# Performance work log

Hardware: AMD Instinct MI355X
Metric: run time of the kernel (lower is better)

The kernel has to match this reference:

```python
import jax, jax.numpy as jnp
import numpy as np
from jax import lax

B, T, C = 64, 512, 512  # time_step == channel required by LayerNorm([T, C]) on [B, C, T]
T2 = T // 2  # downsampled length for scale 1 (conv kernel=2, stride=2)
LN_EPS = 1e-5


def _hardswish(x):
    return x * jnp.clip(x + 3.0, 0.0, 6.0) / 6.0


def _triu_mix(z, W, b):
    # TriU: out[..., i] = Linear_i(z[..., 0:i+1]) == causal lower-triangular mixing
    # z: [B, C, T'], W: [T', T'] (row i holds weights of linear i), b: [T']
    mask = jnp.tril(jnp.ones(W.shape, z.dtype))
    return jnp.einsum('bcj,ij->bci', z, W * mask) + b


def setup_inputs() -> dict:
    key = jax.random.key(0)
    ks = jax.random.split(key, 13)
    s = 0.02
    return {
        'x': jax.random.normal(ks[0], (B, T, C), jnp.float32),
        'ln_gamma': jnp.ones((T, C), jnp.float32),
        'ln_beta': jnp.zeros((T, C), jnp.float32),
        'w1': jax.random.normal(ks[1], (T, T), jnp.float32) * s,
        'b1': jax.random.normal(ks[2], (T,), jnp.float32) * s,
        'w2': jax.random.normal(ks[3], (T, T), jnp.float32) * s,
        'b2': jax.random.normal(ks[4], (T,), jnp.float32) * s,
        'conv_w': jax.random.normal(ks[5], (C, C, 2), jnp.float32) * s,  # OIH
        'conv_b': jax.random.normal(ks[6], (C,), jnp.float32) * s,
        'w3': jax.random.normal(ks[7], (T2, T2), jnp.float32) * s,
        'b3': jax.random.normal(ks[8], (T2,), jnp.float32) * s,
        'w4': jax.random.normal(ks[9], (T2, T2), jnp.float32) * s,
        'b4': jax.random.normal(ks[10], (T2,), jnp.float32) * s,
    }


def reference(x, ln_gamma, ln_beta, w1, b1, w2, b2, conv_w, conv_b, w3, b3, w4, b4):
    xp = jnp.transpose(x, (0, 2, 1))  # [B, C, T]
    # scale 0: LayerNorm over last two dims (C, T jointly), affine weight [T, C] == [C, T] positionally
    mean = jnp.mean(xp, axis=(-2, -1), keepdims=True)
    var = jnp.var(xp, axis=(-2, -1), keepdims=True)
    xn = (xp - mean) / jnp.sqrt(var + LN_EPS) * ln_gamma + ln_beta
    y = _triu_mix(xn, w1, b1)
    y = _hardswish(y)
    y = _triu_mix(y, w2, b2)
    # scale 1: Conv1d(C, C, kernel=2, stride=2) then TriU/Hardswish/TriU on length T/2
    z = lax.conv_general_dilated(xp, conv_w, window_strides=(2,), padding='VALID',
                                 dimension_numbers=('NCH', 'OIH', 'NCH'))
    z = z + conv_b[None, :, None]
    z = _triu_mix(z, w3, b3)
    z = _hardswish(z)
    z = _triu_mix(z, w4, b4)
    return jnp.concatenate([y, z], axis=-1)  # [B, C, T + T/2]
```

## Files before the change

### kernel.cpp

```cpp
#include <hip/hip_runtime.h>
#include <hip/hip_bf16.h>


#define NB 64

typedef __bf16 bf16x8 __attribute__((ext_vector_type(8)));
typedef __bf16 bf16x4 __attribute__((ext_vector_type(4)));
typedef float f32x4 __attribute__((ext_vector_type(4)));

#define AS_GLOBAL __attribute__((address_space(1)))
#define AS_LDS    __attribute__((address_space(3)))

__global__ void pre1_k(const float* __restrict__ x, float* __restrict__ part,
                       const float* __restrict__ w1, const float* __restrict__ w2,
                       const float* __restrict__ w3, const float* __restrict__ w4,
                       const float* __restrict__ cw,
                       __bf16* __restrict__ w1b, __bf16* __restrict__ w2b,
                       __bf16* __restrict__ w3b, __bf16* __restrict__ w4b,
                       __bf16* __restrict__ WtT) {
  if (blockIdx.x < 256) {
    int bb = blockIdx.x;
    int b = bb >> 2, q = bb & 3;
    const float4* xb = (const float4*)(x + (size_t)b * 262144 + (size_t)q * 65536);
    float s = 0.f, ss = 0.f;
    for (int it = 0; it < 64; ++it) {
      float4 v = xb[threadIdx.x + 256 * it];
      s += (v.x + v.y) + (v.z + v.w);
      ss += (v.x * v.x + v.y * v.y) + (v.z * v.z + v.w * v.w);
    }
    __shared__ float ls[256], lss[256];
    ls[threadIdx.x] = s; lss[threadIdx.x] = ss;
    __syncthreads();
    for (int off = 128; off > 0; off >>= 1) {
      if (threadIdx.x < off) {
        ls[threadIdx.x] += ls[threadIdx.x + off];
        lss[threadIdx.x] += lss[threadIdx.x + off];
      }
      __syncthreads();
    }
    if (threadIdx.x == 0) { part[bb * 2] = ls[0]; part[bb * 2 + 1] = lss[0]; }
    return;
  }
  int idx = (blockIdx.x - 256) * 256 + threadIdx.x;
  if (idx < 262144) { int i = idx >> 9, j = idx & 511; w1b[idx] = (__bf16)(j <= i ? w1[idx] : 0.f); return; }
  idx -= 262144;
  if (idx < 262144) { int i = idx >> 9, j = idx & 511; w2b[idx] = (__bf16)(j <= i ? w2[idx] : 0.f); return; }
  idx -= 262144;
  if (idx < 65536) { int i = idx >> 8, j = idx & 255; w3b[idx] = (__bf16)(j <= i ? w3[idx] : 0.f); return; }
  idx -= 65536;
  if (idx < 65536) { int i = idx >> 8, j = idx & 255; w4b[idx] = (__bf16)(j <= i ? w4[idx] : 0.f); return; }
  idx -= 65536;
  int o = idx >> 10, r = idx & 1023;
  int i = r & 511, k = r >> 9;
  WtT[idx] = (__bf16)cw[(size_t)o * 1024 + i * 2 + k];
}

__global__ void stats_final_k(const float* __restrict__ part, float* __restrict__ stats) {
  int b = threadIdx.x;
  if (b < NB) {
    float s = 0.f, ss = 0.f;
    for (int q = 0; q < 4; ++q) { s += part[(b * 4 + q) * 2]; ss += part[(b * 4 + q) * 2 + 1]; }
    float mean = s * (1.f / 262144.f);
    float var = ss * (1.f / 262144.f) - mean * mean;
    stats[b * 2] = mean;
    stats[b * 2 + 1] = rsqrtf(var + 1e-5f);
  }
}

__global__ __launch_bounds__(256) void norm_trans_k(
    const float* __restrict__ x, const float* __restrict__ g,
    const float* __restrict__ be, const float* __restrict__ stats,
    __bf16* __restrict__ XnT, __bf16* __restrict__ xbf) {
  __shared__ float ls[64][65];
  int b = blockIdx.z;
  int bc = blockIdx.x * 64;
  int bt = blockIdx.y * 64;
  int tid = threadIdx.x;
  float mean = stats[b * 2], istd = stats[b * 2 + 1];
  const float* xb = x + (size_t)b * 262144;
  __bf16* xo = xbf + (size_t)b * 262144;
  int r0 = tid >> 4;
  int c4 = (tid & 15) * 4;
#pragma unroll
  for (int p = 0; p < 4; ++p) {
    int t = p * 16 + r0;
    float4 v = *(const float4*)&xb[(size_t)(bt + t) * 512 + bc + c4];
    ls[t][c4] = v.x; ls[t][c4 + 1] = v.y; ls[t][c4 + 2] = v.z; ls[t][c4 + 3] = v.w;
    bf16x4 o;
    o[0] = (__bf16)v.x; o[1] = (__bf16)v.y; o[2] = (__bf16)v.z; o[3] = (__bf16)v.w;
    *(bf16x4*)&xo[(size_t)(bt + t) * 512 + bc + c4] = o;
  }
  __syncthreads();
  int cr = tid >> 3;
  int t0 = (tid & 7) * 8;
  __bf16* xnb = XnT + (size_t)b * 262144;
#pragma unroll
  for (int p = 0; p < 2; ++p) {
    int cg = bc + p * 32 + cr;
    int cl = p * 32 + cr;
    float4 g0 = *(const float4*)&g[(size_t)cg * 512 + bt + t0];
    float4 g1 = *(const float4*)&g[(size_t)cg * 512 + bt + t0 + 4];
    float4 e0 = *(const float4*)&be[(size_t)cg * 512 + bt + t0];
    float4 e1 = *(const float4*)&be[(size_t)cg * 512 + bt + t0 + 4];
    float gv[8] = {g0.x, g0.y, g0.z, g0.w, g1.x, g1.y, g1.z, g1.w};
    float ev[8] = {e0.x, e0.y, e0.z, e0.w, e1.x, e1.y, e1.z, e1.w};
    bf16x8 o;
#pragma unroll
    for (int j = 0; j < 8; ++j) {
      float xh = (ls[t0 + j][cl] - mean) * istd;
      o[j] = (__bf16)(xh * gv[j] + ev[j]);
    }
    *(bf16x8*)&xnb[(size_t)cg * 512 + bt + t0] = o;
  }
}

template <int LGX, bool HSW, bool ROWB, bool COLB, bool OUTBF>
__global__ __launch_bounds__(256, 3) void gemm_mfma_k(
    const __bf16* __restrict__ A, long sAb,
    const __bf16* __restrict__ Bt, long sBb,
    void* __restrict__ Cm, long sCb,
    const float* __restrict__ bias,
    int K, int ldc, int c_off) {
  __shared__ __align__(16) __bf16 As[128 * 64];
  __shared__ __align__(16) __bf16 Bs[128 * 64];
  const int tid = threadIdx.x;
  const int lane = tid & 63, wid = tid >> 6;
  const int wm = (wid >> 1) * 64, wn = (wid & 1) * 64;
  const int lr = lane & 15, lg = lane >> 4;

  const int bid = blockIdx.x + (blockIdx.y << LGX) + (blockIdx.z << (LGX + 2));
  const int nid = ((bid & 7) << (LGX + 5)) | (bid >> 3);
  const int bm = (nid & ((1 << LGX) - 1)) * 128;
  const int bn = ((nid >> LGX) & 3) * 128;
  const int bz = nid >> (LGX + 2);

  const int srg = lane >> 3;
  const int ssrc = ((lane & 7) ^ srg) << 3;

  const __bf16* gA[4];
  const __bf16* gB[4];
#pragma unroll
  for (int p = 0; p < 4; ++p) {
    int row = p * 32 + wid * 8 + srg;
    gA[p] = A + (size_t)bz * sAb + (size_t)(bm + row) * K + ssrc;
    gB[p] = Bt + (size_t)bz * sBb + (size_t)(bn + row) * K + ssrc;
  }

  f32x4 acc[4][4] = {};

  for (int k0 = 0; k0 < K; k0 += 64) {
#pragma unroll
    for (int p = 0; p < 4; ++p) {
      __builtin_amdgcn_global_load_lds(
          (const AS_GLOBAL void*)gA[p],
          (AS_LDS void*)&As[(p * 32 + wid * 8) * 64], 16, 0, 0);
      __builtin_amdgcn_global_load_lds(
          (const AS_GLOBAL void*)gB[p],
          (AS_LDS void*)&Bs[(p * 32 + wid * 8) * 64], 16, 0, 0);
      gA[p] += 64;
      gB[p] += 64;
    }
    __syncthreads();
#pragma unroll
    for (int kk = 0; kk < 64; kk += 32) {
      bf16x8 af[4], bfv[4];
#pragma unroll
      for (int f = 0; f < 4; ++f) {
        int ar = wm + f * 16 + lr;
        af[f] = *(const bf16x8*)&As[ar * 64 + ((kk + lg * 8) ^ ((ar & 7) << 3))];
        int br = wn + f * 16 + lr;
        bfv[f] = *(const bf16x8*)&Bs[br * 64 + ((kk + lg * 8) ^ ((br & 7) << 3))];
      }
#pragma unroll
      for (int i = 0; i < 4; ++i)
#pragma unroll
        for (int j = 0; j < 4; ++j)
          acc[i][j] = __builtin_amdgcn_mfma_f32_16x16x32_bf16(af[i], bfv[j], acc[i][j], 0, 0, 0);
    }
    __syncthreads();
  }

#pragma unroll
  for (int i = 0; i < 4; ++i) {
    int row0 = bm + wm + i * 16 + lg * 4;
    float rb0 = 0.f, rb1 = 0.f, rb2 = 0.f, rb3 = 0.f;
    if (ROWB) { rb0 = bias[row0]; rb1 = bias[row0 + 1]; rb2 = bias[row0 + 2]; rb3 = bias[row0 + 3]; }
#pragma unroll
    for (int j = 0; j < 4; ++j) {
      int col = bn + wn + j * 16 + lr;
      float cbv = COLB ? bias[col] : 0.f;
      float v[4] = {acc[i][j][0] + rb0 + cbv, acc[i][j][1] + rb1 + cbv,
                    acc[i][j][2] + rb2 + cbv, acc[i][j][3] + rb3 + cbv};
      if (HSW) {
#pragma unroll
        for (int r = 0; r < 4; ++r) {
          float u = fminf(fmaxf(v[r] + 3.f, 0.f), 6.f);
          v[r] = v[r] * u * (1.f / 6.f);
        }
      }
      if (OUTBF) {
        __bf16* C = (__bf16*)Cm + (size_t)bz * sCb;
        bf16x4 o;
        o[0] = (__bf16)v[0]; o[1] = (__bf16)v[1]; o[2] = (__bf16)v[2]; o[3] = (__bf16)v[3];
        *(bf16x4*)&C[(size_t)col * ldc + c_off + row0] = o;
      } else {
        float* C = (float*)Cm + (size_t)bz * sCb;
        *(float4*)&C[(size_t)col * ldc + c_off + row0] =
            make_float4(v[0], v[1], v[2], v[3]);
      }
    }
  }
}

extern "C" void kernel_launch(void* const* d_in, const int* in_sizes, int n_in,
                              void* d_out, int out_size, void* d_ws, size_t ws_size,
                              hipStream_t stream) {
  const float* x  = (const float*)d_in[0];
  const float* g  = (const float*)d_in[1];
  const float* be = (const float*)d_in[2];
  const float* w1 = (const float*)d_in[3];
  const float* b1 = (const float*)d_in[4];
  const float* w2 = (const float*)d_in[5];
  const float* b2 = (const float*)d_in[6];
  const float* cw = (const float*)d_in[7];
  const float* cb = (const float*)d_in[8];
  const float* w3 = (const float*)d_in[9];
  const float* b3 = (const float*)d_in[10];
  const float* w4 = (const float*)d_in[11];
  const float* b4 = (const float*)d_in[12];
  float* out = (float*)d_out;

  char* ws = (char*)d_ws;
  float*  stats = (float*)(ws);
  float*  part  = (float*)(ws + 4096);
  __bf16* w1b   = (__bf16*)(ws + (1 << 20));
  __bf16* w2b   = (__bf16*)(ws + (1 << 20) + 524288);
  __bf16* w3b   = (__bf16*)(ws + (2 << 20));
  __bf16* w4b   = (__bf16*)(ws + (2 << 20) + 131072);
  __bf16* WtT   = (__bf16*)(ws + (3 << 20));
  __bf16* xbf   = (__bf16*)(ws + ((size_t)4 << 20));
  __bf16* XnT   = (__bf16*)(ws + ((size_t)36 << 20));
  __bf16* Y1T   = (__bf16*)(ws + ((size_t)68 << 20));
  __bf16* Z1T   = (__bf16*)(ws + ((size_t)100 << 20));
  __bf16* Z3T   = (__bf16*)(ws + ((size_t)116 << 20));

  pre1_k<<<4864, 256, 0, stream>>>(x, part, w1, w2, w3, w4, cw, w1b, w2b, w3b, w4b, WtT);
  stats_final_k<<<1, 64, 0, stream>>>(part, stats);
  norm_trans_k<<<dim3(8, 8, NB), 256, 0, stream>>>(x, g, be, stats, XnT, xbf);

  gemm_mfma_k<2, true, true, false, true><<<dim3(4, 4, NB), 256, 0, stream>>>(
      w1b, 0, XnT, 262144, Y1T, 262144, b1, 512, 512, 0);
  gemm_mfma_k<2, false, true, false, false><<<dim3(4, 4, NB), 256, 0, stream>>>(
      w2b, 0, Y1T, 262144, out, 393216, b2, 512, 768, 0);
  gemm_mfma_k<1, false, false, true, true><<<dim3(2, 4, NB), 256, 0, stream>>>(
      xbf, 262144, WtT, 0, Z1T, 131072, cb, 1024, 256, 0);
  gemm_mfma_k<1, true, true, false, true><<<dim3(2, 4, NB), 256, 0, stream>>>(
      w3b, 0, Z1T, 131072, Z3T, 131072, b3, 256, 256, 0);
  gemm_mfma_k<1, false, true, false, false><<<dim3(2, 4, NB), 256, 0, stream>>>(
      w4b, 0, Z3T, 131072, out, 393216, b4, 256, 768, 512);
}
```

Before: 151.6 us.

## Merge independent kernels into horizontally fused launches and fold stats finalization

The separate stats-finalize kernel is removed, and each normalization block now recomputes mean and inverse std from the partial sums. The bf16 copy of x moves into the statistics pass. The independent conv GEMM and the normalize-transpose step now share one launch, and the paired scale-0 and scale-1 TriU GEMMs are grouped into two combined launches. The aim is to cut launch count and fill the device better by running independent work side by side, at the cost of mixed block types within one grid and the fixed launch-bounds and LDS budget that suits the GEMM.

```diff
diff --git a/kernel.cpp b/kernel.cpp
--- a/kernel.cpp
+++ b/kernel.cpp
@@ -12,6 +12,7 @@
 #define AS_LDS    __attribute__((address_space(3)))
 
 __global__ void pre1_k(const float* __restrict__ x, float* __restrict__ part,
+                       __bf16* __restrict__ xbf,
                        const float* __restrict__ w1, const float* __restrict__ w2,
                        const float* __restrict__ w3, const float* __restrict__ w4,
                        const float* __restrict__ cw,
@@ -21,12 +22,18 @@
   if (blockIdx.x < 256) {
     int bb = blockIdx.x;
     int b = bb >> 2, q = bb & 3;
-    const float4* xb = (const float4*)(x + (size_t)b * 262144 + (size_t)q * 65536);
+    size_t base = (size_t)b * 262144 + (size_t)q * 65536;
+    const float4* xb = (const float4*)(x + base);
+    bf16x4* xo = (bf16x4*)(xbf + base);
     float s = 0.f, ss = 0.f;
     for (int it = 0; it < 64; ++it) {
-      float4 v = xb[threadIdx.x + 256 * it];
+      int idx = threadIdx.x + 256 * it;
+      float4 v = xb[idx];
       s += (v.x + v.y) + (v.z + v.w);
       ss += (v.x * v.x + v.y * v.y) + (v.z * v.z + v.w * v.w);
+      bf16x4 o;
+      o[0] = (__bf16)v.x; o[1] = (__bf16)v.y; o[2] = (__bf16)v.z; o[3] = (__bf16)v.w;
+      xo[idx] = o;
     }
     __shared__ float ls[256], lss[256];
     ls[threadIdx.x] = s; lss[threadIdx.x] = ss;
@@ -55,30 +62,120 @@
   WtT[idx] = (__bf16)cw[(size_t)o * 1024 + i * 2 + k];
 }
 
-__global__ void stats_final_k(const float* __restrict__ part, float* __restrict__ stats) {
-  int b = threadIdx.x;
-  if (b < NB) {
-    float s = 0.f, ss = 0.f;
-    for (int q = 0; q < 4; ++q) { s += part[(b * 4 + q) * 2]; ss += part[(b * 4 + q) * 2 + 1]; }
-    float mean = s * (1.f / 262144.f);
-    float var = ss * (1.f / 262144.f) - mean * mean;
-    stats[b * 2] = mean;
-    stats[b * 2 + 1] = rsqrtf(var + 1e-5f);
-  }
-}
-
-__global__ __launch_bounds__(256) void norm_trans_k(
+template <bool HSW, bool ROWB, bool COLB, bool OUTBF>
+__device__ __forceinline__ void gemm_body(
+    int bid, int lgx, __bf16* As, __bf16* Bs,
+    const __bf16* __restrict__ A, long sAb,
+    const __bf16* __restrict__ Bt, long sBb,
+    void* __restrict__ Cm, long sCb,
+    const float* __restrict__ bias,
+    int K, int ldc, int c_off) {
+  const int tid = threadIdx.x;
+  const int lane = tid & 63, wid = tid >> 6;
+  const int wm = (wid >> 1) * 64, wn = (wid & 1) * 64;
+  const int lr = lane & 15, lg = lane >> 4;
+
+  const int nid = ((bid & 7) << (lgx + 5)) | (bid >> 3);
+  const int bm = (nid & ((1 << lgx) - 1)) * 128;
+  const int bn = ((nid >> lgx) & 3) * 128;
+  const int bz = nid >> (lgx + 2);
+
+  const int srg = lane >> 3;
+  const int ssrc = ((lane & 7) ^ srg) << 3;
+
+  const __bf16* gA[4];
+  const __bf16* gB[4];
+#pragma unroll
+  for (int p = 0; p < 4; ++p) {
+    int row = p * 32 + wid * 8 + srg;
+    gA[p] = A + (size_t)bz * sAb + (size_t)(bm + row) * K + ssrc;
+    gB[p] = Bt + (size_t)bz * sBb + (size_t)(bn + row) * K + ssrc;
+  }
+
+  f32x4 acc[4][4] = {};
+
+  for (int k0 = 0; k0 < K; k0 += 64) {
+#pragma unroll
+    for (int p = 0; p < 4; ++p) {
+      __builtin_amdgcn_global_load_lds(
+          (const AS_GLOBAL void*)gA[p],
+          (AS_LDS void*)&As[(p * 32 + wid * 8) * 64], 16, 0, 0);
+      __builtin_amdgcn_global_load_lds(
+          (const AS_GLOBAL void*)gB[p],
+          (AS_LDS void*)&Bs[(p * 32 + wid * 8) * 64], 16, 0, 0);
+      gA[p] += 64;
+      gB[p] += 64;
+    }
+    __syncthreads();
+#pragma unroll
+    for (int kk = 0; kk < 64; kk += 32) {
+      bf16x8 af[4], bfv[4];
+#pragma unroll
+      for (int f = 0; f < 4; ++f) {
+        int ar = wm + f * 16 + lr;
+        af[f] = *(const bf16x8*)&As[ar * 64 + ((kk + lg * 8) ^ ((ar & 7) << 3))];
+        int br = wn + f * 16 + lr;
+        bfv[f] = *(const bf16x8*)&Bs[br * 64 + ((kk + lg * 8) ^ ((br & 7) << 3))];
+      }
+#pragma unroll
+      for (int i = 0; i < 4; ++i)
+#pragma unroll
+        for (int j = 0; j < 4; ++j)
+          acc[i][j] = __builtin_amdgcn_mfma_f32_16x16x32_bf16(af[i], bfv[j], acc[i][j], 0, 0, 0);
+    }
+    __syncthreads();
+  }
+
+#pragma unroll
+  for (int i = 0; i < 4; ++i) {
+    int row0 = bm + wm + i * 16 + lg * 4;
+    float rb0 = 0.f, rb1 = 0.f, rb2 = 0.f, rb3 = 0.f;
+    if (ROWB) { rb0 = bias[row0]; rb1 = bias[row0 + 1]; rb2 = bias[row0 + 2]; rb3 = bias[row0 + 3]; }
+#pragma unroll
+    for (int j = 0; j < 4; ++j) {
+      int col = bn + wn + j * 16 + lr;
+      float cbv = COLB ? bias[col] : 0.f;
+      float v[4] = {acc[i][j][0] + rb0 + cbv, acc[i][j][1] + rb1 + cbv,
+                    acc[i][j][2] + rb2 + cbv, acc[i][j][3] + rb3 + cbv};
+      if (HSW) {
+#pragma unroll
+        for (int r = 0; r < 4; ++r) {
+          float u = fminf(fmaxf(v[r] + 3.f, 0.f), 6.f);
+          v[r] = v[r] * u * (1.f / 6.f);
+        }
+      }
+      if (OUTBF) {
+        __bf16* C = (__bf16*)Cm + (size_t)bz * sCb;
+        bf16x4 o;
+        o[0] = (__bf16)v[0]; o[1] = (__bf16)v[1]; o[2] = (__bf16)v[2]; o[3] = (__bf16)v[3];
+        *(bf16x4*)&C[(size_t)col * ldc + c_off + row0] = o;
+      } else {
+        float* C = (float*)Cm + (size_t)bz * sCb;
+        *(float4*)&C[(size_t)col * ldc + c_off + row0] =
+            make_float4(v[0], v[1], v[2], v[3]);
+      }
+    }
+  }
+}
+
+__device__ __forceinline__ void norm_body(
+    int bid, char* smem,
     const float* __restrict__ x, const float* __restrict__ g,
-    const float* __restrict__ be, const float* __restrict__ stats,
-    __bf16* __restrict__ XnT, __bf16* __restrict__ xbf) {
-  __shared__ float ls[64][65];
-  int b = blockIdx.z;
-  int bc = blockIdx.x * 64;
-  int bt = blockIdx.y * 64;
+    const float* __restrict__ be, const float* __restrict__ part,
+    __bf16* __restrict__ XnT) {
+  float (*ls)[65] = (float(*)[65])smem;
+  int b = bid >> 6;
+  int r = bid & 63;
+  int bc = (r & 7) * 64;
+  int bt = (r >> 3) * 64;
   int tid = threadIdx.x;
-  float mean = stats[b * 2], istd = stats[b * 2 + 1];
+  float s = 0.f, ss = 0.f;
+#pragma unroll
+  for (int q = 0; q < 4; ++q) { s += part[(b * 4 + q) * 2]; ss += part[(b * 4 + q) * 2 + 1]; }
+  float mean = s * (1.f / 262144.f);
+  float istd = rsqrtf(ss * (1.f / 262144.f) - mean * mean + 1e-5f);
+
   const float* xb = x + (size_t)b * 262144;
-  __bf16* xo = xbf + (size_t)b * 262144;
   int r0 = tid >> 4;
   int c4 = (tid & 15) * 4;
 #pragma unroll
@@ -86,9 +183,6 @@
     int t = p * 16 + r0;
     float4 v = *(const float4*)&xb[(size_t)(bt + t) * 512 + bc + c4];
     ls[t][c4] = v.x; ls[t][c4 + 1] = v.y; ls[t][c4 + 2] = v.z; ls[t][c4 + 3] = v.w;
-    bf16x4 o;
-    o[0] = (__bf16)v.x; o[1] = (__bf16)v.y; o[2] = (__bf16)v.z; o[3] = (__bf16)v.w;
-    *(bf16x4*)&xo[(size_t)(bt + t) * 512 + bc + c4] = o;
   }
   __syncthreads();
   int cr = tid >> 3;
@@ -114,102 +208,56 @@
   }
 }
 
-template <int LGX, bool HSW, bool ROWB, bool COLB, bool OUTBF>
-__global__ __launch_bounds__(256, 3) void gemm_mfma_k(
-    const __bf16* __restrict__ A, long sAb,
-    const __bf16* __restrict__ Bt, long sBb,
-    void* __restrict__ Cm, long sCb,
-    const float* __restrict__ bias,
-    int K, int ldc, int c_off) {
-  __shared__ __align__(16) __bf16 As[128 * 64];
-  __shared__ __align__(16) __bf16 Bs[128 * 64];
-  const int tid = threadIdx.x;
-  const int lane = tid & 63, wid = tid >> 6;
-  const int wm = (wid >> 1) * 64, wn = (wid & 1) * 64;
-  const int lr = lane & 15, lg = lane >> 4;
-
-  const int bid = blockIdx.x + (blockIdx.y << LGX) + (blockIdx.z << (LGX + 2));
-  const int nid = ((bid & 7) << (LGX + 5)) | (bid >> 3);
-  const int bm = (nid & ((1 << LGX) - 1)) * 128;
-  const int bn = ((nid >> LGX) & 3) * 128;
-  const int bz = nid >> (LGX + 2);
-
-  const int srg = lane >> 3;
-  const int ssrc = ((lane & 7) ^ srg) << 3;
-
-  const __bf16* gA[4];
-  const __bf16* gB[4];
-#pragma unroll
-  for (int p = 0; p < 4; ++p) {
-    int row = p * 32 + wid * 8 + srg;
-    gA[p] = A + (size_t)bz * sAb + (size_t)(bm + row) * K + ssrc;
-    gB[p] = Bt + (size_t)bz * sBb + (size_t)(bn + row) * K + ssrc;
-  }
-
-  f32x4 acc[4][4] = {};
-
-  for (int k0 = 0; k0 < K; k0 += 64) {
-#pragma unroll
-    for (int p = 0; p < 4; ++p) {
-      __builtin_amdgcn_global_load_lds(
-          (const AS_GLOBAL void*)gA[p],
-          (AS_LDS void*)&As[(p * 32 + wid * 8) * 64], 16, 0, 0);
-      __builtin_amdgcn_global_load_lds(
-          (const AS_GLOBAL void*)gB[p],
-          (AS_LDS void*)&Bs[(p * 32 + wid * 8) * 64], 16, 0, 0);
-      gA[p] += 64;
-      gB[p] += 64;
-    }
-    __syncthreads();
-#pragma unroll
-    for (int kk = 0; kk < 64; kk += 32) {
-      bf16x8 af[4], bfv[4];
-#pragma unroll
-      for (int f = 0; f < 4; ++f) {
-        int ar = wm + f * 16 + lr;
-        af[f] = *(const bf16x8*)&As[ar * 64 + ((kk + lg * 8) ^ ((ar & 7) << 3))];
-        int br = wn + f * 16 + lr;
-        bfv[f] = *(const bf16x8*)&Bs[br * 64 + ((kk + lg * 8) ^ ((br & 7) << 3))];
-      }
-#pragma unroll
-      for (int i = 0; i < 4; ++i)
-#pragma unroll
-        for (int j = 0; j < 4; ++j)
-          acc[i][j] = __builtin_amdgcn_mfma_f32_16x16x32_bf16(af[i], bfv[j], acc[i][j], 0, 0, 0);
-    }
-    __syncthreads();
-  }
-
-#pragma unroll
-  for (int i = 0; i < 4; ++i) {
-    int row0 = bm + wm + i * 16 + lg * 4;
-    float rb0 = 0.f, rb1 = 0.f, rb2 = 0.f, rb3 = 0.f;
-    if (ROWB) { rb0 = bias[row0]; rb1 = bias[row0 + 1]; rb2 = bias[row0 + 2]; rb3 = bias[row0 + 3]; }
-#pragma unroll
-    for (int j = 0; j < 4; ++j) {
-      int col = bn + wn + j * 16 + lr;
-      float cbv = COLB ? bias[col] : 0.f;
-      float v[4] = {acc[i][j][0] + rb0 + cbv, acc[i][j][1] + rb1 + cbv,
-                    acc[i][j][2] + rb2 + cbv, acc[i][j][3] + rb3 + cbv};
-      if (HSW) {
-#pragma unroll
-        for (int r = 0; r < 4; ++r) {
-          float u = fminf(fmaxf(v[r] + 3.f, 0.f), 6.f);
-          v[r] = v[r] * u * (1.f / 6.f);
-        }
-      }
-      if (OUTBF) {
-        __bf16* C = (__bf16*)Cm + (size_t)bz * sCb;
-        bf16x4 o;
-        o[0] = (__bf16)v[0]; o[1] = (__bf16)v[1]; o[2] = (__bf16)v[2]; o[3] = (__bf16)v[3];
-        *(bf16x4*)&C[(size_t)col * ldc + c_off + row0] = o;
-      } else {
-        float* C = (float*)Cm + (size_t)bz * sCb;
-        *(float4*)&C[(size_t)col * ldc + c_off + row0] =
-            make_float4(v[0], v[1], v[2], v[3]);
-      }
-    }
-  }
+__global__ __launch_bounds__(256, 3) void fused_g3_norm_k(
+    const __bf16* __restrict__ xbf, const __bf16* __restrict__ WtT,
+    __bf16* __restrict__ Z1T, const float* __restrict__ cb,
+    const float* __restrict__ x, const float* __restrict__ g,
+    const float* __restrict__ be, const float* __restrict__ part,
+    __bf16* __restrict__ XnT) {
+  __shared__ __align__(16) char smem[33280];
+  __bf16* As = (__bf16*)smem;
+  __bf16* Bs = (__bf16*)(smem + 16384);
+  int bid = blockIdx.x;
+  if (bid < 512) {
+    gemm_body<false, false, true, true>(bid, 1, As, Bs,
+        xbf, 262144, WtT, 0, Z1T, 131072, cb, 1024, 256, 0);
+  } else {
+    norm_body(bid - 512, smem, x, g, be, part, XnT);
+  }
+}
+
+__global__ __launch_bounds__(256, 3) void fused_g1_g4_k(
+    const __bf16* __restrict__ w1b, const __bf16* __restrict__ XnT,
+    __bf16* __restrict__ Y1T, const float* __restrict__ b1,
+    const __bf16* __restrict__ w3b, const __bf16* __restrict__ Z1T,
+    __bf16* __restrict__ Z3T, const float* __restrict__ b3) {
+  __shared__ __align__(16) char smem[32768];
+  __bf16* As = (__bf16*)smem;
+  __bf16* Bs = (__bf16*)(smem + 16384);
+  int bid = blockIdx.x;
+  if (bid < 1024)
+    gemm_body<true, true, false, true>(bid, 2, As, Bs,
+        w1b, 0, XnT, 262144, Y1T, 262144, b1, 512, 512, 0);
+  else
+    gemm_body<true, true, false, true>(bid - 1024, 1, As, Bs,
+        w3b, 0, Z1T, 131072, Z3T, 131072, b3, 256, 256, 0);
+}
+
+__global__ __launch_bounds__(256, 3) void fused_g2_g5_k(
+    const __bf16* __restrict__ w2b, const __bf16* __restrict__ Y1T,
+    float* __restrict__ out, const float* __restrict__ b2,
+    const __bf16* __restrict__ w4b, const __bf16* __restrict__ Z3T,
+    const float* __restrict__ b4) {
+  __shared__ __align__(16) char smem[32768];
+  __bf16* As = (__bf16*)smem;
+  __bf16* Bs = (__bf16*)(smem + 16384);
+  int bid = blockIdx.x;
+  if (bid < 1024)
+    gemm_body<false, true, false, false>(bid, 2, As, Bs,
+        w2b, 0, Y1T, 262144, out, 393216, b2, 512, 768, 0);
+  else
+    gemm_body<false, true, false, false>(bid - 1024, 1, As, Bs,
+        w4b, 0, Z3T, 131072, out, 393216, b4, 256, 768, 512);
 }
 
 extern "C" void kernel_launch(void* const* d_in, const int* in_sizes, int n_in,
@@ -231,7 +279,6 @@
   float* out = (float*)d_out;
 
   char* ws = (char*)d_ws;
-  float*  stats = (float*)(ws);
   float*  part  = (float*)(ws + 4096);
   __bf16* w1b   = (__bf16*)(ws + (1 << 20));
   __bf16* w2b   = (__bf16*)(ws + (1 << 20) + 524288);
@@ -244,18 +291,9 @@
   __bf16* Z1T   = (__bf16*)(ws + ((size_t)100 << 20));
   __bf16* Z3T   = (__bf16*)(ws + ((size_t)116 << 20));
 
-  pre1_k<<<4864, 256, 0, stream>>>(x, part, w1, w2, w3, w4, cw, w1b, w2b, w3b, w4b, WtT);
-  stats_final_k<<<1, 64, 0, stream>>>(part, stats);
-  norm_trans_k<<<dim3(8, 8, NB), 256, 0, stream>>>(x, g, be, stats, XnT, xbf);
-
-  gemm_mfma_k<2, true, true, false, true><<<dim3(4, 4, NB), 256, 0, stream>>>(
-      w1b, 0, XnT, 262144, Y1T, 262144, b1, 512, 512, 0);
-  gemm_mfma_k<2, false, true, false, false><<<dim3(4, 4, NB), 256, 0, stream>>>(
-      w2b, 0, Y1T, 262144, out, 393216, b2, 512, 768, 0);
-  gemm_mfma_k<1, false, false, true, true><<<dim3(2, 4, NB), 256, 0, stream>>>(
-      xbf, 262144, WtT, 0, Z1T, 131072, cb, 1024, 256, 0);
-  gemm_mfma_k<1, true, true, false, true><<<dim3(2, 4, NB), 256, 0, stream>>>(
-      w3b, 0, Z1T, 131072, Z3T, 131072, b3, 256, 256, 0);
-  gemm_mfma_k<1, false, true, false, false><<<dim3(2, 4, NB), 256, 0, stream>>>(
-      w4b, 0, Z3T, 131072, out, 393216, b4, 256, 768, 512);
-}
+  pre1_k<<<4864, 256, 0, stream>>>(x, part, xbf, w1, w2, w3, w4, cw,
+                                   w1b, w2b, w3b, w4b, WtT);
+  fused_g3_norm_k<<<4608, 256, 0, stream>>>(xbf, WtT, Z1T, cb, x, g, be, part, XnT);
+  fused_g1_g4_k<<<1536, 256, 0, stream>>>(w1b, XnT, Y1T, b1, w3b, Z1T, Z3T, b3);
+  fused_g2_g5_k<<<1536, 256, 0, stream>>>(w2b, Y1T, out, b2, w4b, Z3T, b4);
+}
```

After: 133.0 us. 1.14x faster.
